# Performance work log

Hardware: AMD Instinct MI355X
Metric: run time of the kernel (lower is better)

## Reference

```python
import jax, jax.numpy as jnp
import numpy as np

B, N, H = 16, 8192, 128
TOK_MLP, CH_MLP = 256, 512
EPS = 1e-5


def _layer_norm(z, g, b):
    m = jnp.mean(z, axis=-1, keepdims=True)
    v = jnp.mean(jnp.square(z - m), axis=-1, keepdims=True)
    return (z - m) * jax.lax.rsqrt(v + EPS) * g + b


def setup_inputs() -> dict:
    key = jax.random.key(0)
    ks = jax.random.split(key, 9)
    s = 0.02
    return {
        "x": jax.random.normal(ks[0], (B, N, H), dtype=jnp.float32),
        "ln1_g": jnp.ones((H,), jnp.float32),
        "ln1_b": jnp.zeros((H,), jnp.float32),
        "ln2_g": jnp.ones((H,), jnp.float32),
        "ln2_b": jnp.zeros((H,), jnp.float32),
        "tok_w1": jax.random.normal(ks[1], (N, TOK_MLP), jnp.float32) * s,
        "tok_b1": jnp.zeros((TOK_MLP,), jnp.float32),
        "tok_w2": jax.random.normal(ks[2], (TOK_MLP, N), jnp.float32) * s,
        "tok_b2": jnp.zeros((N,), jnp.float32),
        "ch_w1": jax.random.normal(ks[3], (H, CH_MLP), jnp.float32) * s,
        "ch_b1": jnp.zeros((CH_MLP,), jnp.float32),
        "ch_w2": jax.random.normal(ks[4], (CH_MLP, H), jnp.float32) * s,
        "ch_b2": jnp.zeros((H,), jnp.float32),
    }


def reference(x, ln1_g, ln1_b, ln2_g, ln2_b,
              tok_w1, tok_b1, tok_w2, tok_b2,
              ch_w1, ch_b1, ch_w2, ch_b2):
    # x: [B, N, H]
    y = _layer_norm(x, ln1_g, ln1_b)
    # mask-expand-multiply-sum over dim=2 == reverse (suffix) cumsum over tokens:
    # out[b, j, h] = sum_{i >= j} y[b, i, h]
    y = jnp.flip(jnp.cumsum(jnp.flip(y, axis=1), axis=1), axis=1)  # [B, N, H]
    y = jnp.swapaxes(y, 1, 2)                                      # [B, H, N]
    h = jax.nn.gelu(y @ tok_w1 + tok_b1, approximate=False)        # [B, H, TOK_MLP]
    y = h @ tok_w2 + tok_b2                                        # [B, H, N]
    y = jnp.swapaxes(y, 1, 2)                                      # [B, N, H]
    y = _layer_norm(y, ln2_g, ln2_b)
    h = jax.nn.gelu(y @ ch_w1 + ch_b1, approximate=False)          # [B, N, CH_MLP]
    return h @ ch_w2 + ch_b2                                       # [B, N, H]
```

## Files before the change

kernel.cpp:

```cpp
#include <hip/hip_runtime.h>
#include <math.h>

#define B_ 16
#define N_ 8192
#define H_ 128
#define T_ 256
#define C_ 512

typedef __bf16 bf16x8 __attribute__((ext_vector_type(8)));
typedef __bf16 bf16x4 __attribute__((ext_vector_type(4)));
typedef float f32x4 __attribute__((ext_vector_type(4)));

__device__ __forceinline__ float gelu_f(float x) {
    float p = fmaf(0.044715f * x * x, x, x);
    float e = __expf(-1.5957691216057308f * p);
    return x * __builtin_amdgcn_rcpf(1.f + e);
}

__device__ __forceinline__ unsigned short f2bf(float x) {
    unsigned int u = __float_as_uint(x);
    u = (u + 0x7FFFu + ((u >> 16) & 1u)) >> 16;
    return (unsigned short)u;
}

__device__ __forceinline__ void gl2lds16(const void* g, void* l) {
    __builtin_amdgcn_global_load_lds(
        (const __attribute__((address_space(1))) void*)g,
        (__attribute__((address_space(3))) void*)l,
        16, 0, 0);
}

__global__ void k_w1_scan(const float* __restrict__ psum, float* __restrict__ offs) {
    int t = threadIdx.x;
    const float* p = psum + t * 128;
    float run = 0.f;
    #pragma unroll 8
    for (int c = 0; c < 128; ++c) {
        offs[c * T_ + t] = run;
        run += p[c];
    }
}

__global__ void k_w1_prefix(const float* __restrict__ w1, const float* __restrict__ offs,
                            unsigned short* __restrict__ w1ct) {
    int c = blockIdx.x, t = threadIdx.x;
    float run = offs[c * T_ + t];
    const float* p = w1 + (size_t)c * 64 * T_ + t;
    unsigned int wb[32];
    #pragma unroll
    for (int q = 0; q < 32; ++q) {
        run += p[(size_t)(2 * q) * T_];
        unsigned int lo = f2bf(run);
        run += p[(size_t)(2 * q + 1) * T_];
        wb[q] = lo | ((unsigned int)f2bf(run) << 16);
    }
    char* row = (char*)w1ct + ((size_t)t * N_ + c * 64) * 2;
    int key = (t & 7) << 4;
    #pragma unroll
    for (int pc = 0; pc < 8; ++pc) {
        int4 v = { (int)wb[4*pc], (int)wb[4*pc+1], (int)wb[4*pc+2], (int)wb[4*pc+3] };
        *(int4*)(row + ((pc * 16) ^ key)) = v;
    }
}

__global__ void k_packs(const float* __restrict__ w2, unsigned short* __restrict__ w2t,
                        const float* __restrict__ cw1, const float* __restrict__ cw2,
                        unsigned short* __restrict__ w1p, unsigned short* __restrict__ w2p,
                        const float* __restrict__ w1tok, float* __restrict__ psum) {
    __shared__ float ld[64 * 68];
    int tid = threadIdx.x;
    if (blockIdx.y < 4) {
        int nt = blockIdx.x, tt = blockIdx.y;
        int n0 = nt * 64, t0 = tt * 64;
        #pragma unroll
        for (int rnd = 0; rnd < 4; ++rnd) {
            int idx = tid + rnd * 256;
            int tr = idx >> 4, nc = idx & 15;
            float4 v = *(const float4*)(w2 + (size_t)(t0 + tr) * N_ + n0 + nc * 4);
            *(float4*)&ld[tr * 68 + nc * 4] = v;
        }
        __syncthreads();
        int n = tid >> 2, q = tid & 3;
        int key = (n & 7) << 4;
        unsigned int wb[8];
        #pragma unroll
        for (int j = 0; j < 8; ++j) {
            float a = ld[(q * 16 + 2 * j) * 68 + n];
            float b = ld[(q * 16 + 2 * j + 1) * 68 + n];
            wb[j] = (unsigned int)f2bf(a) | ((unsigned int)f2bf(b) << 16);
        }
        char* row = (char*)w2t + (size_t)(n0 + n) * 512 + t0 * 2;
        int4 v0 = { (int)wb[0], (int)wb[1], (int)wb[2], (int)wb[3] };
        int4 v1 = { (int)wb[4], (int)wb[5], (int)wb[6], (int)wb[7] };
        *(int4*)(row + ((q * 32) ^ key)) = v0;
        *(int4*)(row + ((q * 32 + 16) ^ key)) = v1;
    } else if (blockIdx.y < 8) {
        int e = ((blockIdx.y - 4) * 128 + blockIdx.x) * 256 + tid;
        if (e < 65536) {
            int c = e >> 13, t = e & 8191;
            int n = t >> 7, j = t & 127;
            int k = j ^ ((n & 7) << 3);
            int hid = c * 64 + n;
            w1p[e] = f2bf(cw1[(size_t)k * C_ + hid]);
        } else {
            int e2 = e - 65536;
            int c = e2 >> 13, t = e2 & 8191;
            int n = t >> 6, j = t & 63;
            int k = j ^ ((n & 7) << 3);
            w2p[e2] = f2bf(cw2[(size_t)(c * 64 + k) * H_ + n]);
        }
    } else {
        int c = blockIdx.x, t = tid;
        const float* p = w1tok + (size_t)c * 64 * T_ + t;
        float s = 0.f;
        #pragma unroll 8
        for (int r = 0; r < 64; ++r) s += p[(size_t)r * T_];
        psum[t * 128 + c] = s;
    }
}

#define T1_YS 0
#define T1_WS 16384
#define T1_LN 81920

__global__ __launch_bounds__(1024, 1)
void k_tok1(const float* __restrict__ x, const float* __restrict__ lg,
            const float* __restrict__ lb, const unsigned short* __restrict__ w1ct,
            float* __restrict__ P) {
    __shared__ __align__(16) char sm[115712];
    float* lnb = (float*)(sm + T1_LN);
    int kk = blockIdx.x, b = blockIdx.y;
    int tid = threadIdx.x;
    int w = tid >> 6, lane = tid & 63;
    int lr = lane & 15, lk = lane >> 4;
    int mg = w >> 2, ng = w & 3;
    const char* wbg = (const char*)w1ct;
    int kbase = kk * 512;

    int rI = tid >> 4, lI = tid & 15;
    int hII = tid >> 3, segII = tid & 7;
    const float* xbase = x + ((size_t)b * N_ + kbase) * H_;

    float4 g0 = *(const float4*)(lg + lI * 8);
    float4 g1 = *(const float4*)(lg + lI * 8 + 4);
    float4 c0 = *(const float4*)(lb + lI * 8);
    float4 c1 = *(const float4*)(lb + lI * 8 + 4);

    f32x4 acc[2][4];
    #pragma unroll
    for (int i = 0; i < 2; ++i)
        #pragma unroll
        for (int j = 0; j < 4; ++j) acc[i][j] = (f32x4){0.f, 0.f, 0.f, 0.f};

    float4 xa, xb;
    auto XLOAD = [&](int t) {
        const float* p = xbase + (size_t)(t * 64 + rI) * H_ + lI * 8;
        xa = *(const float4*)p;
        xb = *(const float4*)(p + 4);
    };
    auto LNW = [&]() {
        float s1 = xa.x + xa.y + xa.z + xa.w + xb.x + xb.y + xb.z + xb.w;
        float s2 = xa.x*xa.x + xa.y*xa.y + xa.z*xa.z + xa.w*xa.w
                 + xb.x*xb.x + xb.y*xb.y + xb.z*xb.z + xb.w*xb.w;
        #pragma unroll
        for (int off = 1; off < 16; off <<= 1) {
            s1 += __shfl_xor(s1, off);
            s2 += __shfl_xor(s2, off);
        }
        float mean = s1 * (1.f / 128.f);
        float rstd = rsqrtf(s2 * (1.f / 128.f) - mean * mean + 1e-5f);
        float4 o0, o1;
        o0.x = (xa.x - mean) * rstd * g0.x + c0.x;
        o0.y = (xa.y - mean) * rstd * g0.y + c0.y;
        o0.z = (xa.z - mean) * rstd * g0.z + c0.z;
        o0.w = (xa.w - mean) * rstd * g0.w + c0.w;
        o1.x = (xb.x - mean) * rstd * g1.x + c1.x;
        o1.y = (xb.y - mean) * rstd * g1.y + c1.y;
        o1.z = (xb.z - mean) * rstd * g1.z + c1.z;
        o1.w = (xb.w - mean) * rstd * g1.w + c1.w;
        *(float4*)&lnb[rI * 132 + lI * 8]     = o0;
        *(float4*)&lnb[rI * 132 + lI * 8 + 4] = o1;
    };
    auto COLW = [&]() {
        unsigned int d[4];
        #pragma unroll
        for (int j = 0; j < 4; ++j) {
            float a = lnb[(segII * 8 + 2 * j) * 132 + hII];
            float c = lnb[(segII * 8 + 2 * j + 1) * 132 + hII];
            d[j] = (unsigned int)f2bf(a) | ((unsigned int)f2bf(c) << 16);
        }
        int4 v = { (int)d[0], (int)d[1], (int)d[2], (int)d[3] };
        *(int4*)(sm + T1_YS + hII * 128 + ((segII * 16) ^ ((hII & 7) << 4))) = v;
    };
    auto STAGEW = [&](int s, char* buf) {
        int n0 = kbase + s * 64;
        #pragma unroll
        for (int rnd = 0; rnd < 2; ++rnd) {
            int idx = tid + rnd * 1024;
            int tr = idx >> 3, pp = idx & 7;
            gl2lds16(wbg + ((size_t)tr * N_ + n0) * 2 + pp * 16, buf + idx * 16);
        }
    };

    STAGEW(0, sm + T1_WS);
    XLOAD(0);

    for (int s = 0; s < 8; ++s) {
        LNW();
        if (s < 7) XLOAD(s + 1);
        __syncthreads();
        COLW();
        __syncthreads();
        if (s < 7) STAGEW(s + 1, sm + T1_WS + ((s + 1) & 1) * 32768);
        const char* wsb = sm + T1_WS + (s & 1) * 32768;
        #pragma unroll
        for (int ks = 0; ks < 2; ++ks) {
            bf16x8 af[2], bfr[4];
            #pragma unroll
            for (int i = 0; i < 2; ++i) {
                int h = mg * 32 + i * 16 + lr;
                af[i] = *(const bf16x8*)(sm + T1_YS + h * 128 + ((ks * 64 + lk * 16) ^ ((h & 7) << 4)));
            }
            #pragma unroll
            for (int j = 0; j < 4; ++j) {
                int t = ng * 64 + j * 16 + lr;
                bfr[j] = *(const bf16x8*)(wsb + t * 128 + ((ks * 64 + lk * 16) ^ ((t & 7) << 4)));
            }
            #pragma unroll
            for (int i = 0; i < 2; ++i)
                #pragma unroll
                for (int j = 0; j < 4; ++j)
                    acc[i][j] = __builtin_amdgcn_mfma_f32_16x16x32_bf16(af[i], bfr[j], acc[i][j], 0, 0, 0);
        }
        __syncthreads();
    }

    float* Pb = P + ((size_t)(b * 16 + kk)) * (H_ * T_);
    #pragma unroll
    for (int i = 0; i < 2; ++i)
        #pragma unroll
        for (int j = 0; j < 4; ++j) {
            int t = ng * 64 + j * 16 + lr;
            #pragma unroll
            for (int r = 0; r < 4; ++r) {
                int h = mg * 32 + i * 16 + lk * 4 + r;
                Pb[h * T_ + t] = acc[i][j][r];
            }
        }
}

__global__ void k_tok1_fin(const float* __restrict__ P, const float* __restrict__ b1,
                           unsigned short* __restrict__ g1b) {
    int fid = blockIdx.x * 256 + threadIdx.x;
    int base = fid * 4;
    int b = base >> 15, rem = base & 32767;
    int h = rem >> 8, t = rem & 255;
    const float* Pb = P + (size_t)b * 16 * 32768 + rem;
    float4 a = *(const float4*)Pb;
    #pragma unroll
    for (int kk = 1; kk < 16; ++kk) {
        float4 p = *(const float4*)(Pb + (size_t)kk * 32768);
        a.x += p.x; a.y += p.y; a.z += p.z; a.w += p.w;
    }
    float4 bb = *(const float4*)(b1 + t);
    unsigned int lo = (unsigned int)f2bf(gelu_f(a.x + bb.x)) | ((unsigned int)f2bf(gelu_f(a.y + bb.y)) << 16);
    unsigned int hi = (unsigned int)f2bf(gelu_f(a.z + bb.z)) | ((unsigned int)f2bf(gelu_f(a.w + bb.w)) << 16);
    char* row = (char*)g1b + (size_t)(b * H_ + h) * 512;
    uint2 v = { lo, hi };
    *(uint2*)(row + ((t * 2) ^ ((h & 7) << 4))) = v;
}

#define F_YS 0
#define F_HS 0
#define F_W2 32768
#define F_W1 49152

__global__ __launch_bounds__(512, 4)
void k_tok2mlp(const unsigned short* __restrict__ g1b, const unsigned short* __restrict__ w2t,
               const float* __restrict__ tb2, const float* __restrict__ lg,
               const float* __restrict__ lb, const unsigned short* __restrict__ w1p,
               const unsigned short* __restrict__ w2p, const float* __restrict__ b1g,
               const float* __restrict__ b2g, float* __restrict__ out) {
    __shared__ __align__(16) char sm[65536];
    int nt = blockIdx.x, b = blockIdx.y;
    int tid = threadIdx.x;
    int w = tid >> 6, lane = tid & 63;
    int lr = lane & 15, lk = lane >> 4;
    const char* ab = (const char*)w2t + (size_t)(nt * 128) * 512;
    const char* gb = (const char*)g1b + (size_t)b * H_ * 512;
    const char* w1b = (const char*)w1p;
    const char* w2b = (const char*)w2p;

    f32x4 acc[8];
    #pragma unroll
    for (int g = 0; g < 8; ++g) acc[g] = (f32x4){0.f, 0.f, 0.f, 0.f};

    int arow = w * 16 + lr;
    int akey = (arow & 7) << 4;

    #pragma unroll
    for (int rnd = 0; rnd < 2; ++rnd) {
        int idx = tid + rnd * 512;
        int row = idx >> 3, p = idx & 7;
        gl2lds16(ab + (size_t)row * 512 + p * 16, sm + row * 128 + p * 16);
        gl2lds16(gb + (size_t)row * 512 + p * 16, sm + 16384 + row * 128 + p * 16);
    }
    __syncthreads();

    for (int q = 0; q < 4; ++q) {
        const char* cur = sm + (q & 1) * 32768;
        if (q < 3) {
            char* nxt = sm + ((q + 1) & 1) * 32768;
            #pragma unroll
            for (int rnd = 0; rnd < 2; ++rnd) {
                int idx = tid + rnd * 512;
                int row = idx >> 3, p = idx & 7;
                gl2lds16(ab + (size_t)row * 512 + (q + 1) * 128 + p * 16, nxt + row * 128 + p * 16);
                gl2lds16(gb + (size_t)row * 512 + (q + 1) * 128 + p * 16, nxt + 16384 + row * 128 + p * 16);
            }
        }
        __builtin_amdgcn_s_setprio(1);
        #pragma unroll
        for (int ks = 0; ks < 2; ++ks) {
            bf16x8 af = *(const bf16x8*)(cur + arow * 128 + ((ks * 64 + lk * 16) ^ akey));
            #pragma unroll
            for (int g = 0; g < 8; ++g) {
                int hrow = g * 16 + lr;
                bf16x8 bf_ = *(const bf16x8*)(cur + 16384 + hrow * 128 + ((ks * 64 + lk * 16) ^ ((hrow & 7) << 4)));
                acc[g] = __builtin_amdgcn_mfma_f32_16x16x32_bf16(af, bf_, acc[g], 0, 0, 0);
            }
        }
        __builtin_amdgcn_s_setprio(0);
        __syncthreads();
    }

    float gam[8], bet[8];
    #pragma unroll
    for (int g = 0; g < 8; ++g) { gam[g] = lg[g * 16 + lr]; bet[g] = lb[g * 16 + lr]; }

    #pragma unroll
    for (int j = 0; j < 2; ++j) {
        gl2lds16(w1b + w * 2048 + j * 1024 + lane * 16, sm + F_W1 + w * 2048 + j * 1024);
        gl2lds16(w2b + w * 2048 + j * 1024 + lane * 16, sm + F_W2 + w * 2048 + j * 1024);
    }

    #pragma unroll
    for (int r = 0; r < 4; ++r) {
        int row = w * 16 + lk * 4 + r;
        float bias2 = tb2[nt * 128 + row];
        float vals[8];
        float s = 0.f, ss = 0.f;
        #pragma unroll
        for (int g = 0; g < 8; ++g) {
            float v = acc[g][r] + bias2;
            vals[g] = v; s += v; ss += v * v;
        }
        #pragma unroll
        for (int off = 8; off; off >>= 1) { s += __shfl_xor(s, off); ss += __shfl_xor(ss, off); }
        float mean = s * (1.f / 128.f);
        float rstd = rsqrtf(ss * (1.f / 128.f) - mean * mean + 1e-5f);
        int key = (row & 7) << 4;
        char* orow = sm + F_YS + row * 256;
        #pragma unroll
        for (int g = 0; g < 8; ++g) {
            float v = (vals[g] - mean) * rstd * gam[g] + bet[g];
            *(unsigned short*)(orow + (((g * 16 + lr) * 2) ^ key)) = f2bf(v);
        }
    }
    __syncthreads();

    int mg = w >> 1, ng = w & 1;
    int key = (lr & 7) << 4;

    bf16x8 yfrag[2][4];
    #pragma unroll
    for (int m = 0; m < 2; ++m) {
        int yrow = (2 * mg + m) * 16 + lr;
        #pragma unroll
        for (int kc = 0; kc < 4; ++kc)
            yfrag[m][kc] = *(const bf16x8*)(sm + F_YS + yrow * 256 + ((kc * 64 + lk * 16) ^ key));
    }
    __syncthreads();

    f32x4 oacc[2][4];
    #pragma unroll
    for (int m = 0; m < 2; ++m)
        #pragma unroll
        for (int n = 0; n < 4; ++n) oacc[m][n] = (f32x4){0.f, 0.f, 0.f, 0.f};

    for (int c = 0; c < 8; ++c) {
        f32x4 hacc[2][2];
        #pragma unroll
        for (int n = 0; n < 2; ++n) {
            float4 bv4 = *(const float4*)(b1g + c * 64 + (2 * ng + n) * 16 + lk * 4);
            f32x4 iv = { bv4.x, bv4.y, bv4.z, bv4.w };
            hacc[0][n] = iv;
            hacc[1][n] = iv;
        }
        __builtin_amdgcn_s_setprio(1);
        #pragma unroll
        for (int kc = 0; kc < 4; ++kc) {
            int ko = kc * 64 + lk * 16;
            bf16x8 b0 = *(const bf16x8*)(sm + F_W1 + ((2 * ng) * 16 + lr) * 256 + (ko ^ key));
            bf16x8 b1 = *(const bf16x8*)(sm + F_W1 + ((2 * ng + 1) * 16 + lr) * 256 + (ko ^ key));
            hacc[0][0] = __builtin_amdgcn_mfma_f32_16x16x32_bf16(b0, yfrag[0][kc], hacc[0][0], 0, 0, 0);
            hacc[0][1] = __builtin_amdgcn_mfma_f32_16x16x32_bf16(b1, yfrag[0][kc], hacc[0][1], 0, 0, 0);
            hacc[1][0] = __builtin_amdgcn_mfma_f32_16x16x32_bf16(b0, yfrag[1][kc], hacc[1][0], 0, 0, 0);
            hacc[1][1] = __builtin_amdgcn_mfma_f32_16x16x32_bf16(b1, yfrag[1][kc], hacc[1][1], 0, 0, 0);
        }
        __builtin_amdgcn_s_setprio(0);
        #pragma unroll
        for (int m = 0; m < 2; ++m)
            #pragma unroll
            for (int n = 0; n < 2; ++n) {
                int tok = (2 * mg + m) * 16 + lr;
                int hid0 = (2 * ng + n) * 16 + lk * 4;
                bf16x4 pv;
                pv[0] = (__bf16)gelu_f(hacc[m][n][0]);
                pv[1] = (__bf16)gelu_f(hacc[m][n][1]);
                pv[2] = (__bf16)gelu_f(hacc[m][n][2]);
                pv[3] = (__bf16)gelu_f(hacc[m][n][3]);
                *(bf16x4*)(sm + F_HS + tok * 128 + ((hid0 * 2) ^ ((tok & 7) << 4))) = pv;
            }
        __syncthreads();
        if (c < 7) {
            #pragma unroll
            for (int j = 0; j < 2; ++j)
                gl2lds16(w1b + (c + 1) * 16384 + w * 2048 + j * 1024 + lane * 16,
                         sm + F_W1 + w * 2048 + j * 1024);
        }
        __builtin_amdgcn_s_setprio(1);
        #pragma unroll
        for (int kc = 0; kc < 2; ++kc) {
            int ko = kc * 64 + lk * 16;
            int t0 = (2 * mg) * 16 + lr, t1 = (2 * mg + 1) * 16 + lr;
            bf16x8 a0 = *(const bf16x8*)(sm + F_HS + t0 * 128 + (ko ^ ((t0 & 7) << 4)));
            bf16x8 a1 = *(const bf16x8*)(sm + F_HS + t1 * 128 + (ko ^ ((t1 & 7) << 4)));
            #pragma unroll
            for (int n = 0; n < 4; ++n) {
                bf16x8 bb = *(const bf16x8*)(sm + F_W2 + ((ng * 4 + n) * 16 + lr) * 128 + (ko ^ key));
                oacc[0][n] = __builtin_amdgcn_mfma_f32_16x16x32_bf16(a0, bb, oacc[0][n], 0, 0, 0);
                oacc[1][n] = __builtin_amdgcn_mfma_f32_16x16x32_bf16(a1, bb, oacc[1][n], 0, 0, 0);
            }
        }
        __builtin_amdgcn_s_setprio(0);
        __syncthreads();
        if (c < 7) {
            #pragma unroll
            for (int j = 0; j < 2; ++j)
                gl2lds16(w2b + (c + 1) * 16384 + w * 2048 + j * 1024 + lane * 16,
                         sm + F_W2 + w * 2048 + j * 1024);
        }
    }

    size_t rbase = (size_t)(b * 64 + nt) * 128;
    #pragma unroll
    for (int n = 0; n < 4; ++n) {
        int ch = (ng * 4 + n) * 16 + lr;
        float bv = b2g[ch];
        #pragma unroll
        for (int m = 0; m < 2; ++m)
            #pragma unroll
            for (int r = 0; r < 4; ++r) {
                size_t row = rbase + (2 * mg + m) * 16 + lk * 4 + r;
                out[row * H_ + ch] = oacc[m][n][r] + bv;
            }
    }
}

extern "C" void kernel_launch(void* const* d_in, const int* in_sizes, int n_in,
                              void* d_out, int out_size, void* d_ws, size_t ws_size,
                              hipStream_t stream) {
    const float* x      = (const float*)d_in[0];
    const float* ln1_g  = (const float*)d_in[1];
    const float* ln1_b  = (const float*)d_in[2];
    const float* ln2_g  = (const float*)d_in[3];
    const float* ln2_b  = (const float*)d_in[4];
    const float* tok_w1 = (const float*)d_in[5];
    const float* tok_b1 = (const float*)d_in[6];
    const float* tok_w2 = (const float*)d_in[7];
    const float* tok_b2 = (const float*)d_in[8];
    const float* ch_w1  = (const float*)d_in[9];
    const float* ch_b1  = (const float*)d_in[10];
    const float* ch_w2  = (const float*)d_in[11];
    const float* ch_b2  = (const float*)d_in[12];
    float* out = (float*)d_out;
    float* ws  = (float*)d_ws;

    float* psum = ws;
    float* offs = ws + 32768;
    unsigned short* w1ct = (unsigned short*)(ws + 65536);
    unsigned short* w2t  = (unsigned short*)(ws + 1114112);
    unsigned short* w1p  = (unsigned short*)(ws + 2162688);
    unsigned short* w2p  = (unsigned short*)(ws + 2195456);
    unsigned short* g1b  = (unsigned short*)(ws + 2228224);
    float* P             = ws + 2490368;

    k_packs<<<dim3(128, 9), dim3(256), 0, stream>>>(tok_w2, w2t, ch_w1, ch_w2, w1p, w2p,
                                                    tok_w1, psum);
    k_w1_scan<<<dim3(1), dim3(256), 0, stream>>>(psum, offs);
    k_w1_prefix<<<dim3(128), dim3(256), 0, stream>>>(tok_w1, offs, w1ct);
    k_tok1<<<dim3(16, 16), dim3(1024), 0, stream>>>(x, ln1_g, ln1_b, w1ct, P);
    k_tok1_fin<<<dim3(512), dim3(256), 0, stream>>>(P, tok_b1, g1b);
    k_tok2mlp<<<dim3(64, 16), dim3(512), 0, stream>>>(g1b, w2t, tok_b2, ln2_g, ln2_b,
                                                      w1p, w2p, ch_b1, ch_b2, out);
}
```

Baseline: 118.0 us.

## Double token tile per block in fused token-MLP2/channel-MLP kernel

Each block of k_tok2mlp now covers 256 tokens with 1024 threads instead of 128 tokens with 512 threads, so the grid is halved to 32x16. The goal is to reuse each staged tile of the GELU activations and the channel-MLP weights across twice as many tokens, cutting global and L2 traffic for those operands. LDS grows to 96KB and launch bounds drop to one block per CU. That costs latency hiding, and with only 512 blocks the scheduling is coarser.

```diff
diff --git a/kernel.cpp b/kernel.cpp
--- a/kernel.cpp
+++ b/kernel.cpp
@@ -270,23 +270,24 @@
     *(uint2*)(row + ((t * 2) ^ ((h & 7) << 4))) = v;
 }
 
+#define F2_BUF 49152
 #define F_YS 0
 #define F_HS 0
-#define F_W2 32768
-#define F_W1 49152
-
-__global__ __launch_bounds__(512, 4)
+#define F_W1 65536
+#define F_W2 81920
+
+__global__ __launch_bounds__(1024, 1)
 void k_tok2mlp(const unsigned short* __restrict__ g1b, const unsigned short* __restrict__ w2t,
                const float* __restrict__ tb2, const float* __restrict__ lg,
                const float* __restrict__ lb, const unsigned short* __restrict__ w1p,
                const unsigned short* __restrict__ w2p, const float* __restrict__ b1g,
                const float* __restrict__ b2g, float* __restrict__ out) {
-    __shared__ __align__(16) char sm[65536];
+    __shared__ __align__(16) char sm[98304];
     int nt = blockIdx.x, b = blockIdx.y;
     int tid = threadIdx.x;
     int w = tid >> 6, lane = tid & 63;
     int lr = lane & 15, lk = lane >> 4;
-    const char* ab = (const char*)w2t + (size_t)(nt * 128) * 512;
+    const char* ab = (const char*)w2t + (size_t)(nt * 256) * 512;
     const char* gb = (const char*)g1b + (size_t)b * H_ * 512;
     const char* w1b = (const char*)w1p;
     const char* w2b = (const char*)w2p;
@@ -298,27 +299,25 @@
     int arow = w * 16 + lr;
     int akey = (arow & 7) << 4;
 
-    #pragma unroll
-    for (int rnd = 0; rnd < 2; ++rnd) {
-        int idx = tid + rnd * 512;
-        int row = idx >> 3, p = idx & 7;
-        gl2lds16(ab + (size_t)row * 512 + p * 16, sm + row * 128 + p * 16);
-        gl2lds16(gb + (size_t)row * 512 + p * 16, sm + 16384 + row * 128 + p * 16);
-    }
+    auto STAGEQ = [&](int q, char* buf) {
+        #pragma unroll
+        for (int rnd = 0; rnd < 2; ++rnd) {
+            int idx = tid + rnd * 1024;
+            int row = idx >> 3, p = idx & 7;
+            gl2lds16(ab + (size_t)row * 512 + q * 128 + p * 16, buf + row * 128 + p * 16);
+        }
+        {
+            int row = tid >> 3, p = tid & 7;
+            gl2lds16(gb + (size_t)row * 512 + q * 128 + p * 16, buf + 32768 + row * 128 + p * 16);
+        }
+    };
+
+    STAGEQ(0, sm);
     __syncthreads();
 
     for (int q = 0; q < 4; ++q) {
-        const char* cur = sm + (q & 1) * 32768;
-        if (q < 3) {
-            char* nxt = sm + ((q + 1) & 1) * 32768;
-            #pragma unroll
-            for (int rnd = 0; rnd < 2; ++rnd) {
-                int idx = tid + rnd * 512;
-                int row = idx >> 3, p = idx & 7;
-                gl2lds16(ab + (size_t)row * 512 + (q + 1) * 128 + p * 16, nxt + row * 128 + p * 16);
-                gl2lds16(gb + (size_t)row * 512 + (q + 1) * 128 + p * 16, nxt + 16384 + row * 128 + p * 16);
-            }
-        }
+        const char* cur = sm + (q & 1) * F2_BUF;
+        if (q < 3) STAGEQ(q + 1, sm + ((q + 1) & 1) * F2_BUF);
         __builtin_amdgcn_s_setprio(1);
         #pragma unroll
         for (int ks = 0; ks < 2; ++ks) {
@@ -326,7 +325,7 @@
             #pragma unroll
             for (int g = 0; g < 8; ++g) {
                 int hrow = g * 16 + lr;
-                bf16x8 bf_ = *(const bf16x8*)(cur + 16384 + hrow * 128 + ((ks * 64 + lk * 16) ^ ((hrow & 7) << 4)));
+                bf16x8 bf_ = *(const bf16x8*)(cur + 32768 + hrow * 128 + ((ks * 64 + lk * 16) ^ ((hrow & 7) << 4)));
                 acc[g] = __builtin_amdgcn_mfma_f32_16x16x32_bf16(af, bf_, acc[g], 0, 0, 0);
             }
         }
@@ -338,16 +337,13 @@
     #pragma unroll
     for (int g = 0; g < 8; ++g) { gam[g] = lg[g * 16 + lr]; bet[g] = lb[g * 16 + lr]; }
 
-    #pragma unroll
-    for (int j = 0; j < 2; ++j) {
-        gl2lds16(w1b + w * 2048 + j * 1024 + lane * 16, sm + F_W1 + w * 2048 + j * 1024);
-        gl2lds16(w2b + w * 2048 + j * 1024 + lane * 16, sm + F_W2 + w * 2048 + j * 1024);
-    }
+    gl2lds16(w1b + tid * 16, sm + F_W1 + tid * 16);
+    gl2lds16(w2b + tid * 16, sm + F_W2 + tid * 16);
 
     #pragma unroll
     for (int r = 0; r < 4; ++r) {
         int row = w * 16 + lk * 4 + r;
-        float bias2 = tb2[nt * 128 + row];
+        float bias2 = tb2[nt * 256 + row];
         float vals[8];
         float s = 0.f, ss = 0.f;
         #pragma unroll
@@ -423,12 +419,8 @@
                 *(bf16x4*)(sm + F_HS + tok * 128 + ((hid0 * 2) ^ ((tok & 7) << 4))) = pv;
             }
         __syncthreads();
-        if (c < 7) {
-            #pragma unroll
-            for (int j = 0; j < 2; ++j)
-                gl2lds16(w1b + (c + 1) * 16384 + w * 2048 + j * 1024 + lane * 16,
-                         sm + F_W1 + w * 2048 + j * 1024);
-        }
+        if (c < 7)
+            gl2lds16(w1b + (c + 1) * 16384 + tid * 16, sm + F_W1 + tid * 16);
         __builtin_amdgcn_s_setprio(1);
         #pragma unroll
         for (int kc = 0; kc < 2; ++kc) {
@@ -445,15 +437,11 @@
         }
         __builtin_amdgcn_s_setprio(0);
         __syncthreads();
-        if (c < 7) {
-            #pragma unroll
-            for (int j = 0; j < 2; ++j)
-                gl2lds16(w2b + (c + 1) * 16384 + w * 2048 + j * 1024 + lane * 16,
-                         sm + F_W2 + w * 2048 + j * 1024);
-        }
-    }
-
-    size_t rbase = (size_t)(b * 64 + nt) * 128;
+        if (c < 7)
+            gl2lds16(w2b + (c + 1) * 16384 + tid * 16, sm + F_W2 + tid * 16);
+    }
+
+    size_t rbase = (size_t)(b * 32 + nt) * 256;
     #pragma unroll
     for (int n = 0; n < 4; ++n) {
         int ch = (ng * 4 + n) * 16 + lr;
@@ -502,6 +490,6 @@
     k_w1_prefix<<<dim3(128), dim3(256), 0, stream>>>(tok_w1, offs, w1ct);
     k_tok1<<<dim3(16, 16), dim3(1024), 0, stream>>>(x, ln1_g, ln1_b, w1ct, P);
     k_tok1_fin<<<dim3(512), dim3(256), 0, stream>>>(P, tok_b1, g1b);
-    k_tok2mlp<<<dim3(64, 16), dim3(512), 0, stream>>>(g1b, w2t, tok_b2, ln2_g, ln2_b,
-                                                      w1p, w2p, ch_b1, ch_b2, out);
-}
+    k_tok2mlp<<<dim3(32, 16), dim3(1024), 0, stream>>>(g1b, w2t, tok_b2, ln2_g, ln2_b,
+                                                       w1p, w2p, ch_b1, ch_b2, out);
+}
```

Result: slower. 123.6 us (+4.8%).

## Fold w1 scan into prefix kernel and read channel-MLP weights from global

Applied to the files above, without the earlier changes.

Removes the single-block k_w1_scan launch; each k_w1_prefix block now recomputes its own starting offset by summing the preceding per-chunk partial sums. In k_tok2mlp the channel-MLP weights are no longer staged into LDS. MFMA B-fragments are loaded directly from global memory, and the GELU hidden tile is double-buffered in LDS so one of the two barriers per chunk can be dropped. This cuts a launch and some synchronization. The cost is redundant prefix sums, and weight fragments that are re-read from global or L2 by every wave instead of coming from shared memory.

```diff
diff --git a/kernel.cpp b/kernel.cpp
--- a/kernel.cpp
+++ b/kernel.cpp
@@ -30,21 +30,12 @@
         16, 0, 0);
 }
 
-__global__ void k_w1_scan(const float* __restrict__ psum, float* __restrict__ offs) {
-    int t = threadIdx.x;
-    const float* p = psum + t * 128;
-    float run = 0.f;
-    #pragma unroll 8
-    for (int c = 0; c < 128; ++c) {
-        offs[c * T_ + t] = run;
-        run += p[c];
-    }
-}
-
-__global__ void k_w1_prefix(const float* __restrict__ w1, const float* __restrict__ offs,
+__global__ void k_w1_prefix(const float* __restrict__ w1, const float* __restrict__ psum,
                             unsigned short* __restrict__ w1ct) {
     int c = blockIdx.x, t = threadIdx.x;
-    float run = offs[c * T_ + t];
+    const float* pp = psum + t * 128;
+    float run = 0.f;
+    for (int i = 0; i < c; ++i) run += pp[i];
     const float* p = w1 + (size_t)c * 64 * T_ + t;
     unsigned int wb[32];
     #pragma unroll
@@ -271,9 +262,6 @@
 }
 
 #define F_YS 0
-#define F_HS 0
-#define F_W2 32768
-#define F_W1 49152
 
 __global__ __launch_bounds__(512, 4)
 void k_tok2mlp(const unsigned short* __restrict__ g1b, const unsigned short* __restrict__ w2t,
@@ -339,12 +327,6 @@
     for (int g = 0; g < 8; ++g) { gam[g] = lg[g * 16 + lr]; bet[g] = lb[g * 16 + lr]; }
 
     #pragma unroll
-    for (int j = 0; j < 2; ++j) {
-        gl2lds16(w1b + w * 2048 + j * 1024 + lane * 16, sm + F_W1 + w * 2048 + j * 1024);
-        gl2lds16(w2b + w * 2048 + j * 1024 + lane * 16, sm + F_W2 + w * 2048 + j * 1024);
-    }
-
-    #pragma unroll
     for (int r = 0; r < 4; ++r) {
         int row = w * 16 + lk * 4 + r;
         float bias2 = tb2[nt * 128 + row];
@@ -389,6 +371,9 @@
         for (int n = 0; n < 4; ++n) oacc[m][n] = (f32x4){0.f, 0.f, 0.f, 0.f};
 
     for (int c = 0; c < 8; ++c) {
+        char* hsb = sm + (c & 1) * 16384;
+        const char* w1c = w1b + c * 16384;
+        const char* w2c = w2b + c * 16384;
         f32x4 hacc[2][2];
         #pragma unroll
         for (int n = 0; n < 2; ++n) {
@@ -401,8 +386,8 @@
         #pragma unroll
         for (int kc = 0; kc < 4; ++kc) {
             int ko = kc * 64 + lk * 16;
-            bf16x8 b0 = *(const bf16x8*)(sm + F_W1 + ((2 * ng) * 16 + lr) * 256 + (ko ^ key));
-            bf16x8 b1 = *(const bf16x8*)(sm + F_W1 + ((2 * ng + 1) * 16 + lr) * 256 + (ko ^ key));
+            bf16x8 b0 = *(const bf16x8*)(w1c + ((2 * ng) * 16 + lr) * 256 + (ko ^ key));
+            bf16x8 b1 = *(const bf16x8*)(w1c + ((2 * ng + 1) * 16 + lr) * 256 + (ko ^ key));
             hacc[0][0] = __builtin_amdgcn_mfma_f32_16x16x32_bf16(b0, yfrag[0][kc], hacc[0][0], 0, 0, 0);
             hacc[0][1] = __builtin_amdgcn_mfma_f32_16x16x32_bf16(b1, yfrag[0][kc], hacc[0][1], 0, 0, 0);
             hacc[1][0] = __builtin_amdgcn_mfma_f32_16x16x32_bf16(b0, yfrag[1][kc], hacc[1][0], 0, 0, 0);
@@ -420,37 +405,24 @@
                 pv[1] = (__bf16)gelu_f(hacc[m][n][1]);
                 pv[2] = (__bf16)gelu_f(hacc[m][n][2]);
                 pv[3] = (__bf16)gelu_f(hacc[m][n][3]);
-                *(bf16x4*)(sm + F_HS + tok * 128 + ((hid0 * 2) ^ ((tok & 7) << 4))) = pv;
-            }
-        __syncthreads();
-        if (c < 7) {
-            #pragma unroll
-            for (int j = 0; j < 2; ++j)
-                gl2lds16(w1b + (c + 1) * 16384 + w * 2048 + j * 1024 + lane * 16,
-                         sm + F_W1 + w * 2048 + j * 1024);
-        }
+                *(bf16x4*)(hsb + tok * 128 + ((hid0 * 2) ^ ((tok & 7) << 4))) = pv;
+            }
+        __syncthreads();
         __builtin_amdgcn_s_setprio(1);
         #pragma unroll
         for (int kc = 0; kc < 2; ++kc) {
             int ko = kc * 64 + lk * 16;
             int t0 = (2 * mg) * 16 + lr, t1 = (2 * mg + 1) * 16 + lr;
-            bf16x8 a0 = *(const bf16x8*)(sm + F_HS + t0 * 128 + (ko ^ ((t0 & 7) << 4)));
-            bf16x8 a1 = *(const bf16x8*)(sm + F_HS + t1 * 128 + (ko ^ ((t1 & 7) << 4)));
+            bf16x8 a0 = *(const bf16x8*)(hsb + t0 * 128 + (ko ^ ((t0 & 7) << 4)));
+            bf16x8 a1 = *(const bf16x8*)(hsb + t1 * 128 + (ko ^ ((t1 & 7) << 4)));
             #pragma unroll
             for (int n = 0; n < 4; ++n) {
-                bf16x8 bb = *(const bf16x8*)(sm + F_W2 + ((ng * 4 + n) * 16 + lr) * 128 + (ko ^ key));
+                bf16x8 bb = *(const bf16x8*)(w2c + ((ng * 4 + n) * 16 + lr) * 128 + (ko ^ key));
                 oacc[0][n] = __builtin_amdgcn_mfma_f32_16x16x32_bf16(a0, bb, oacc[0][n], 0, 0, 0);
                 oacc[1][n] = __builtin_amdgcn_mfma_f32_16x16x32_bf16(a1, bb, oacc[1][n], 0, 0, 0);
             }
         }
         __builtin_amdgcn_s_setprio(0);
-        __syncthreads();
-        if (c < 7) {
-            #pragma unroll
-            for (int j = 0; j < 2; ++j)
-                gl2lds16(w2b + (c + 1) * 16384 + w * 2048 + j * 1024 + lane * 16,
-                         sm + F_W2 + w * 2048 + j * 1024);
-        }
     }
 
     size_t rbase = (size_t)(b * 64 + nt) * 128;
@@ -488,7 +460,6 @@
     float* ws  = (float*)d_ws;
 
     float* psum = ws;
-    float* offs = ws + 32768;
     unsigned short* w1ct = (unsigned short*)(ws + 65536);
     unsigned short* w2t  = (unsigned short*)(ws + 1114112);
     unsigned short* w1p  = (unsigned short*)(ws + 2162688);
@@ -498,8 +469,7 @@
 
     k_packs<<<dim3(128, 9), dim3(256), 0, stream>>>(tok_w2, w2t, ch_w1, ch_w2, w1p, w2p,
                                                     tok_w1, psum);
-    k_w1_scan<<<dim3(1), dim3(256), 0, stream>>>(psum, offs);
-    k_w1_prefix<<<dim3(128), dim3(256), 0, stream>>>(tok_w1, offs, w1ct);
+    k_w1_prefix<<<dim3(128), dim3(256), 0, stream>>>(tok_w1, psum, w1ct);
     k_tok1<<<dim3(16, 16), dim3(1024), 0, stream>>>(x, ln1_g, ln1_b, w1ct, P);
     k_tok1_fin<<<dim3(512), dim3(256), 0, stream>>>(P, tok_b1, g1b);
     k_tok2mlp<<<dim3(64, 16), dim3(512), 0, stream>>>(g1b, w2t, tok_b2, ln2_g, ln2_b,
```

Measured after the change: 136.5 us. 15.7% more time.
